# Kernel tuning notes

Hardware: AMD Instinct MI355X
Metric: run time of the kernel (lower is better)

Reference implementation:

```python
import jax, jax.numpy as jnp
import numpy as np
import itertools

B, N, C, D = 2, 150000, 64, 128  # samples, points/sample, channels, voxel grid extent
EPS = 1e-4  # BatchNormBlock eps
# 3x3x3 submanifold kernel offsets (27 taps)
OFFS = jnp.array(list(itertools.product((-1, 0, 1), repeat=3)), dtype=jnp.int32)  # [27,3]


def setup_inputs() -> dict:
    key = jax.random.key(0)
    k1, k2 = jax.random.split(key)
    rng = np.random.default_rng(0)
    # unique voxel coordinates per sample on a D^3 grid
    pos = np.stack([
        np.stack(np.unravel_index(rng.choice(D ** 3, size=N, replace=False), (D, D, D)), axis=-1)
        for _ in range(B)
    ]).astype(np.int32)  # [B,N,3]
    feats = jax.random.normal(k1, (B, N, C), jnp.float32)
    # 4 submanifold convs (2 residual blocks x 2 convs), fan-in scaled
    Ws = jax.random.normal(k2, (4, 27, C, C), jnp.float32) / np.sqrt(27 * C)
    gammas = jnp.ones((4, C), jnp.float32)
    betas = jnp.zeros((4, C), jnp.float32)
    return {"feats": feats, "Ws": Ws, "gammas": gammas, "betas": betas, "pos": jnp.asarray(pos)}


def _build_lut(pos_b):  # pos_b: [N,3] int32 -> dense hash grid [D^3] of point index or -1
    code = (pos_b[:, 0] * D + pos_b[:, 1]) * D + pos_b[:, 2]
    return jnp.full((D ** 3,), -1, jnp.int32).at[code].set(jnp.arange(N, dtype=jnp.int32))


def _subconv(x, lut_b, pos_b, W):
    # submanifold sparse conv: per kernel tap, gather neighbor features and GEMM
    # x:[N,C], lut_b:[D^3], pos_b:[N,3], W:[27,Cin,Cout]
    def step(acc, kw):
        d, Wk = kw
        npos = pos_b + d  # [N,3]
        valid = jnp.all((npos >= 0) & (npos < D), axis=-1)
        code = (npos[:, 0] * D + npos[:, 1]) * D + npos[:, 2]
        nidx = lut_b[jnp.where(valid, code, 0)]
        valid = valid & (nidx >= 0)
        g = jnp.where(valid[:, None], x[jnp.clip(nidx, 0, N - 1)], 0.0)  # [N,Cin]
        return acc + g @ Wk, None

    acc0 = jnp.zeros((x.shape[0], W.shape[-1]), x.dtype)
    acc, _ = jax.lax.scan(step, acc0, (OFFS, W))
    return acc


def _bn_relu(x, g, b):
    # BatchNormBlock (train mode, biased var over all concatenated points) + ReLU
    mu = x.mean(axis=(0, 1))
    var = jnp.mean(jnp.square(x - mu), axis=(0, 1))
    return jax.nn.relu((x - mu) * jax.lax.rsqrt(var + EPS) * g + b)


def reference(feats, Ws, gammas, betas, pos):
    lut = jax.vmap(_build_lut)(pos)  # [B, D^3]
    conv = jax.vmap(_subconv, in_axes=(0, 0, 0, None))
    x = feats
    for blk in range(2):  # conv_block_reps ResidualBlocks (NIN is Identity since nIn==nOut)
        out1 = x
        h = _bn_relu(x, gammas[2 * blk], betas[2 * blk])
        h = conv(h, lut, pos, Ws[2 * blk])
        h = _bn_relu(h, gammas[2 * blk + 1], betas[2 * blk + 1])
        out2 = conv(h, lut, pos, Ws[2 * blk + 1])
        x = out1 + out2
    return x
```

## Files before the change

### kernel.cpp

```cpp
#include <hip/hip_runtime.h>
#include <stdint.h>

#define DGRID 128
#define D3 (DGRID * DGRID * DGRID)
#define NBATCH 2
#define NPTS 150000
#define NROWS (NBATCH * NPTS)
#define NPAD 300032
#define ZROW NROWS
#define NCBLK (NPAD / 128)
#define NCELLS 8192
#define EPSBN 1e-4f

typedef __attribute__((ext_vector_type(8))) short s16x8;
typedef __attribute__((ext_vector_type(4))) float f32x4;

static __device__ __forceinline__ uint32_t f2bf_rne(float f) {
  uint32_t b = __float_as_uint(f);
  return (b + 0x7FFFu + ((b >> 16) & 1u)) >> 16;
}

static __device__ __forceinline__ uint32_t pkbf(float lo, float hi) {
  uint32_t r;
  asm("v_cvt_pk_bf16_f32 %0, %1, %2" : "=v"(r) : "v"(lo), "v"(hi));
  return r;
}

static __device__ __forceinline__ f32x4 mfma16(uint4 a, uint4 b, f32x4 c) {
  return __builtin_amdgcn_mfma_f32_16x16x32_bf16(
      __builtin_bit_cast(s16x8, a), __builtin_bit_cast(s16x8, b), c, 0, 0, 0);
}

static __device__ __forceinline__ uint4 bnrelu_frag(uint4 u, float4 aL, float4 aH,
                                                    float4 bL, float4 bH) {
  float y0, y1;
  uint4 o;
  y0 = fmaxf(fmaf(__uint_as_float(u.x << 16), aL.x, bL.x), 0.f);
  y1 = fmaxf(fmaf(__uint_as_float(u.x & 0xFFFF0000u), aL.y, bL.y), 0.f);
  o.x = pkbf(y0, y1);
  y0 = fmaxf(fmaf(__uint_as_float(u.y << 16), aL.z, bL.z), 0.f);
  y1 = fmaxf(fmaf(__uint_as_float(u.y & 0xFFFF0000u), aL.w, bL.w), 0.f);
  o.y = pkbf(y0, y1);
  y0 = fmaxf(fmaf(__uint_as_float(u.z << 16), aH.x, bH.x), 0.f);
  y1 = fmaxf(fmaf(__uint_as_float(u.z & 0xFFFF0000u), aH.y, bH.y), 0.f);
  o.z = pkbf(y0, y1);
  y0 = fmaxf(fmaf(__uint_as_float(u.w << 16), aH.z, bH.z), 0.f);
  y1 = fmaxf(fmaf(__uint_as_float(u.w & 0xFFFF0000u), aH.w, bH.w), 0.f);
  o.w = pkbf(y0, y1);
  return o;
}

__global__ void k_scatter(const int* __restrict__ pos, int* __restrict__ lut) {
  int g = blockIdx.x * blockDim.x + threadIdx.x;
  if (g >= NROWS) return;
  int b = g / NPTS;
  int i = g - b * NPTS;
  lut[(size_t)b * D3 + (pos[3 * g] * DGRID + pos[3 * g + 1]) * DGRID + pos[3 * g + 2]] = i;
}

__global__ void k_cellcount(const int* __restrict__ pos, int* __restrict__ cnt) {
  int g = blockIdx.x * blockDim.x + threadIdx.x;
  if (g >= NROWS) return;
  int b = g / NPTS;
  int cid = (b << 12) | ((pos[3 * g] >> 3) << 8) | ((pos[3 * g + 1] >> 3) << 4) |
            (pos[3 * g + 2] >> 3);
  atomicAdd(&cnt[cid], 1);
}

__global__ void k_scan(const int* __restrict__ cnt, int* __restrict__ cstart) {
  __shared__ int s[1024];
  int tid = threadIdx.x;
  int e[8];
  int sum = 0;
#pragma unroll
  for (int j = 0; j < 8; j++) {
    int v = cnt[tid * 8 + j];
    e[j] = sum;
    sum += v;
  }
  s[tid] = sum;
  __syncthreads();
  for (int off = 1; off < 1024; off <<= 1) {
    int t = (tid >= off) ? s[tid - off] : 0;
    __syncthreads();
    s[tid] += t;
    __syncthreads();
  }
  int base = tid ? s[tid - 1] : 0;
#pragma unroll
  for (int j = 0; j < 8; j++) cstart[tid * 8 + j] = base + e[j];
}

__global__ void k_bucket(const int* __restrict__ pos, const int* __restrict__ cstart,
                         int* __restrict__ fill, int* __restrict__ perm,
                         int* __restrict__ iperm) {
  int g = blockIdx.x * blockDim.x + threadIdx.x;
  if (g >= NROWS) return;
  int b = g / NPTS;
  int cid = (b << 12) | ((pos[3 * g] >> 3) << 8) | ((pos[3 * g + 1] >> 3) << 4) |
            (pos[3 * g + 2] >> 3);
  int slot = cstart[cid] + atomicAdd(&fill[cid], 1);
  perm[slot] = g;
  iperm[g] = slot;
}

__global__ void k_nbr_s(const int* __restrict__ pos, const int* __restrict__ lut,
                        const int* __restrict__ perm, const int* __restrict__ iperm,
                        int* __restrict__ nbr) {
  int s = blockIdx.x * blockDim.x + threadIdx.x;
  if (s >= NPAD) return;
  if (s >= NROWS) {
#pragma unroll
    for (int t = 0; t < 27; ++t) nbr[(size_t)t * NPAD + s] = ZROW;
    return;
  }
  int g = perm[s];
  int b = g / NPTS;
  int x = pos[3 * g], y = pos[3 * g + 1], z = pos[3 * g + 2];
  const int* L = lut + (size_t)b * D3;
  const int* ip = iperm + (size_t)b * NPTS;
#pragma unroll
  for (int t = 0; t < 27; ++t) {
    int nx = x + t / 9 - 1;
    int ny = y + (t / 3) % 3 - 1;
    int nz = z + t % 3 - 1;
    int v = ZROW;
    if ((unsigned)nx < DGRID && (unsigned)ny < DGRID && (unsigned)nz < DGRID) {
      int n = L[(nx * DGRID + ny) * DGRID + nz];
      if (n >= 0) v = ip[n];
    }
    nbr[(size_t)t * NPAD + s] = v;
  }
}

__global__ void k_wpack(const float* __restrict__ Ws, uint4* __restrict__ Wfrag) {
  int e = blockIdx.x * 256 + threadIdx.x;
  if (e >= 4 * 27 * 512) return;
  int lane = e & 63, nb = (e >> 6) & 3, s = (e >> 8) & 1, tt = e >> 9;
  int kb = s * 32 + (lane >> 4) * 8;
  int cout = nb * 16 + (lane & 15);
  const float* src = Ws + (size_t)tt * 4096;
  uint32_t p[4];
#pragma unroll
  for (int j = 0; j < 4; ++j) {
    uint32_t lo = f2bf_rne(src[(kb + 2 * j) * 64 + cout]);
    uint32_t hi = f2bf_rne(src[(kb + 2 * j + 1) * 64 + cout]);
    p[j] = (hi << 16) | lo;
  }
  uint4 o;
  o.x = p[0]; o.y = p[1]; o.z = p[2]; o.w = p[3];
  Wfrag[e] = o;
}

__global__ void k_stats2(const float* __restrict__ part, int nblk,
                         const float* __restrict__ gamma, const float* __restrict__ beta,
                         float* __restrict__ chanp, int cid) {
  __shared__ float s[512];
  int c = threadIdx.x & 63, q = threadIdx.x >> 6;
  float sm = 0.f, sq = 0.f;
  for (int rb = q; rb < nblk; rb += 4) {
    sm += part[rb * 128 + c];
    sq += part[rb * 128 + 64 + c];
  }
  s[threadIdx.x] = sm;
  s[256 + threadIdx.x] = sq;
  __syncthreads();
  if (q == 0) {
    sm = s[c] + s[64 + c] + s[128 + c] + s[192 + c];
    sq = s[256 + c] + s[320 + c] + s[384 + c] + s[448 + c];
    float mean = sm / (float)NROWS;
    float var = sq / (float)NROWS - mean * mean;
    float a = gamma[cid * 64 + c] * rsqrtf(var + EPSBN);
    chanp[cid * 128 + c] = a;
    chanp[cid * 128 + 64 + c] = beta[cid * 64 + c] - mean * a;
  }
}

__global__ void k_cast(const float* __restrict__ feats, const int* __restrict__ perm,
                       uint4* __restrict__ f0, float* __restrict__ part) {
  __shared__ float sred[2][4][64];
  int tid = threadIdx.x, wv = tid >> 6, lane = tid & 63;
  int oct = tid & 7;
  float sm[8], sq[8];
#pragma unroll
  for (int j = 0; j < 8; j++) sm[j] = sq[j] = 0.f;
#pragma unroll 1
  for (int it = 0; it < 8; it++) {
    int g = blockIdx.x * 2048 + it * 256 + tid;
    int s = g >> 3;
    uint4 o = (uint4){0u, 0u, 0u, 0u};
    if (s < NROWS) {
      int src = perm[s];
      const float* X = feats + (size_t)src * 64 + oct * 8;
      float4 x0 = *(const float4*)X;
      float4 x1 = *(const float4*)(X + 4);
      sm[0] += x0.x; sq[0] += x0.x * x0.x;
      sm[1] += x0.y; sq[1] += x0.y * x0.y;
      sm[2] += x0.z; sq[2] += x0.z * x0.z;
      sm[3] += x0.w; sq[3] += x0.w * x0.w;
      sm[4] += x1.x; sq[4] += x1.x * x1.x;
      sm[5] += x1.y; sq[5] += x1.y * x1.y;
      sm[6] += x1.z; sq[6] += x1.z * x1.z;
      sm[7] += x1.w; sq[7] += x1.w * x1.w;
      o.x = pkbf(x0.x, x0.y);
      o.y = pkbf(x0.z, x0.w);
      o.z = pkbf(x1.x, x1.y);
      o.w = pkbf(x1.z, x1.w);
    }
    f0[g] = o;
  }
#pragma unroll
  for (int j = 0; j < 8; j++) {
    sm[j] += __shfl_xor(sm[j], 8);  sq[j] += __shfl_xor(sq[j], 8);
    sm[j] += __shfl_xor(sm[j], 16); sq[j] += __shfl_xor(sq[j], 16);
    sm[j] += __shfl_xor(sm[j], 32); sq[j] += __shfl_xor(sq[j], 32);
  }
  if (lane < 8) {
#pragma unroll
    for (int j = 0; j < 8; j++) {
      sred[0][wv][lane * 8 + j] = sm[j];
      sred[1][wv][lane * 8 + j] = sq[j];
    }
  }
  __syncthreads();
  if (tid < 64) {
    float s0 = 0.f, s1 = 0.f;
#pragma unroll
    for (int w = 0; w < 4; w++) {
      s0 += sred[0][w][tid];
      s1 += sred[1][w][tid];
    }
    part[blockIdx.x * 128 + tid] = s0;
    part[blockIdx.x * 128 + 64 + tid] = s1;
  }
}

__global__ void k_hb(const uint4* __restrict__ x, const float* __restrict__ chanp,
                     int cid, uint4* __restrict__ h) {
  int tid = threadIdx.x;
  int c0 = (tid & 7) * 8;
  const float* cp = chanp + cid * 128;
  float4 aL = *(const float4*)(cp + c0);
  float4 aH = *(const float4*)(cp + c0 + 4);
  float4 bL = *(const float4*)(cp + 64 + c0);
  float4 bH = *(const float4*)(cp + 64 + c0 + 4);
#pragma unroll 1
  for (int it = 0; it < 8; it++) {
    int g = blockIdx.x * 2048 + it * 256 + tid;
    int row = g >> 3;
    uint4 o = (uint4){0u, 0u, 0u, 0u};
    if (row < NROWS) o = bnrelu_frag(x[g], aL, aH, bL, bH);
    h[g] = o;
  }
}

#define PH(T, AC, NIC)                                                      \
  {                                                                         \
    _Pragma("unroll") for (int s = 0; s < 2; s++)                           \
      _Pragma("unroll") for (int rt = 0; rt < 2; rt++)                      \
        _Pragma("unroll") for (int nb = 0; nb < 4; nb++)                    \
          acc[rt][nb] = mfma16(AC[rt][s], wb[s * 4 + nb], acc[rt][nb]);     \
    _Pragma("unroll") for (int rt = 0; rt < 2; rt++) {                      \
      const uint4* hp = src + (size_t)NIC[rt] * 8 + lkg;                    \
      AC[rt][0] = hp[0];                                                    \
      AC[rt][1] = hp[4];                                                    \
    }                                                                       \
    {                                                                       \
      int tn = (T) + 4 <= 26 ? (T) + 4 : 26;                                \
      NIC[0] = nbp[(size_t)tn * NPAD];                                      \
      NIC[1] = nbp[(size_t)tn * NPAD + 16];                                 \
    }                                                                       \
    {                                                                       \
      int tw = (T) + 1 <= 26 ? (T) + 1 : 26;                                \
      const uint4* wp = Wf + (size_t)tw * 512 + lane;                       \
      _Pragma("unroll") for (int i = 0; i < 8; i++) wb[i] = wp[i * 64];     \
    }                                                                       \
  }

__global__ __launch_bounds__(256) void k_conv(
    const uint4* __restrict__ src, const uint4* __restrict__ Wf,
    const int* __restrict__ nbr,
    const uint4* __restrict__ resb, uint4* __restrict__ outb,
    float* __restrict__ outf, const int* __restrict__ operm,
    float* __restrict__ part, int do_stats) {
  __shared__ char smem[19456];
  int tid = threadIdx.x, wv = tid >> 6, lane = tid & 63;
  int bid = (int)blockIdx.x;
  int sbid = (bid & 7) * (NCBLK / 8) + (bid >> 3);
  int tbase = (sbid * 4 + wv) * 32;
  int lrow = lane & 15, lkg = lane >> 4;

  f32x4 acc[2][4];
#pragma unroll
  for (int i = 0; i < 2; i++)
#pragma unroll
    for (int j = 0; j < 4; j++) acc[i][j] = (f32x4){0.f, 0.f, 0.f, 0.f};

  const int* nbp = nbr + tbase + lrow;
  int niE[2], niO[2];
  uint4 aE[2][2], aO[2][2], wb[8];
  {
    int p0[2], p1[2];
    p0[0] = nbp[0];
    p0[1] = nbp[16];
    p1[0] = nbp[NPAD];
    p1[1] = nbp[NPAD + 16];
    niE[0] = nbp[(size_t)2 * NPAD];
    niE[1] = nbp[(size_t)2 * NPAD + 16];
    niO[0] = nbp[(size_t)3 * NPAD];
    niO[1] = nbp[(size_t)3 * NPAD + 16];
#pragma unroll
    for (int rt = 0; rt < 2; rt++) {
      const uint4* hp = src + (size_t)p0[rt] * 8 + lkg;
      aE[rt][0] = hp[0];
      aE[rt][1] = hp[4];
    }
#pragma unroll
    for (int rt = 0; rt < 2; rt++) {
      const uint4* hp = src + (size_t)p1[rt] * 8 + lkg;
      aO[rt][0] = hp[0];
      aO[rt][1] = hp[4];
    }
    const uint4* wp = Wf + lane;
#pragma unroll
    for (int i = 0; i < 8; i++) wb[i] = wp[i * 64];
  }

#pragma unroll 1
  for (int t = 0; t < 26; t += 2) {
    PH(t, aE, niE)
    PH(t + 1, aO, niO)
  }
  PH(26, aE, niE)

  float sm4[4] = {0.f, 0.f, 0.f, 0.f}, sq4[4] = {0.f, 0.f, 0.f, 0.f};
  float* slab = (float*)smem + wv * 1088;
  float* sred = (float*)(smem + 17408);
#pragma unroll 1
  for (int rt = 0; rt < 2; rt++) {
#pragma unroll
    for (int nb = 0; nb < 4; nb++)
#pragma unroll
      for (int r = 0; r < 4; r++)
        slab[(lkg * 4 + r) * 68 + nb * 16 + lrow] = acc[rt][nb][r];
#pragma unroll
    for (int j = 0; j < 4; j++) {
      int row = tbase + rt * 16 + j * 4 + lkg;
      float4 vv = *(float4*)&slab[(j * 4 + lkg) * 68 + lrow * 4];
      bool live = row < NROWS;
      if (resb && live) {
        uint2 rb = *(const uint2*)((const char*)resb + (size_t)row * 128 + lrow * 8);
        vv.x += __uint_as_float(rb.x << 16);
        vv.y += __uint_as_float(rb.x & 0xFFFF0000u);
        vv.z += __uint_as_float(rb.y << 16);
        vv.w += __uint_as_float(rb.y & 0xFFFF0000u);
      }
      if (outb) {
        uint2 ob = (uint2){0u, 0u};
        if (live) {
          ob.x = pkbf(vv.x, vv.y);
          ob.y = pkbf(vv.z, vv.w);
        }
        *(uint2*)((char*)outb + (size_t)row * 128 + lrow * 8) = ob;
      }
      if (outf && live) {
        int orow = operm[row];
        *(float4*)(outf + (size_t)orow * 64 + lrow * 4) = vv;
      }
      if (live) {
        sm4[0] += vv.x; sq4[0] += vv.x * vv.x;
        sm4[1] += vv.y; sq4[1] += vv.y * vv.y;
        sm4[2] += vv.z; sq4[2] += vv.z * vv.z;
        sm4[3] += vv.w; sq4[3] += vv.w * vv.w;
      }
    }
  }
  if (do_stats) {
#pragma unroll
    for (int k = 0; k < 4; k++) {
      sm4[k] += __shfl_xor(sm4[k], 16); sq4[k] += __shfl_xor(sq4[k], 16);
      sm4[k] += __shfl_xor(sm4[k], 32); sq4[k] += __shfl_xor(sq4[k], 32);
    }
    if (lane < 16) {
#pragma unroll
      for (int k = 0; k < 4; k++) {
        sred[wv * 64 + lane * 4 + k] = sm4[k];
        sred[256 + wv * 64 + lane * 4 + k] = sq4[k];
      }
    }
    __syncthreads();
    if (tid < 64) {
      float s0 = 0.f, s1 = 0.f;
#pragma unroll
      for (int w = 0; w < 4; w++) {
        s0 += sred[w * 64 + tid];
        s1 += sred[256 + w * 64 + tid];
      }
      part[bid * 128 + tid] = s0;
      part[bid * 128 + 64 + tid] = s1;
    }
  }
}

extern "C" void kernel_launch(void* const* d_in, const int* in_sizes, int n_in,
                              void* d_out, int out_size, void* d_ws, size_t ws_size,
                              hipStream_t stream) {
  const float* feats = (const float*)d_in[0];
  const float* Ws = (const float*)d_in[1];
  const float* gammas = (const float*)d_in[2];
  const float* betas = (const float*)d_in[3];
  const int* pos = (const int*)d_in[4];
  float* out = (float*)d_out;

  char* w = (char*)d_ws;
  auto alloc = [&](size_t b) {
    char* p = w;
    w += (b + 255) & ~(size_t)255;
    return p;
  };
  int* nbr = (int*)alloc((size_t)27 * NPAD * 4);
  uint4* Wfrag = (uint4*)alloc((size_t)4 * 27 * 512 * 16);
  float* part = (float*)alloc((size_t)NCBLK * 128 * 4);
  float* chanp = (float*)alloc((size_t)4 * 128 * 4);
  int* perm = (int*)alloc((size_t)NPAD * 4);
  int* iperm = (int*)alloc((size_t)NROWS * 4);
  int* ccnt = (int*)alloc((size_t)NCELLS * 4);
  int* cfill = (int*)alloc((size_t)NCELLS * 4);
  int* cstart = (int*)alloc((size_t)NCELLS * 4);
  uint4* f0 = (uint4*)alloc((size_t)NPAD * 128);
  uint4* x1 = (uint4*)alloc((size_t)NPAD * 128);
  uint4* h = (uint4*)alloc((size_t)NPAD * 128);
  char* reg0 = alloc((size_t)NPAD * 128);
  uint4* c1 = (uint4*)reg0;
  int* lut = (int*)reg0;

  hipMemsetAsync(lut, 0xFF, (size_t)NBATCH * D3 * 4, stream);
  hipMemsetAsync(ccnt, 0, (size_t)NCELLS * 8, stream);
  int gpts = (NROWS + 255) / 256;
  k_scatter<<<gpts, 256, 0, stream>>>(pos, lut);
  k_cellcount<<<gpts, 256, 0, stream>>>(pos, ccnt);
  k_scan<<<1, 1024, 0, stream>>>(ccnt, cstart);
  k_bucket<<<gpts, 256, 0, stream>>>(pos, cstart, cfill, perm, iperm);
  k_nbr_s<<<NPAD / 256, 256, 0, stream>>>(pos, lut, perm, iperm, nbr);
  k_wpack<<<216, 256, 0, stream>>>(Ws, Wfrag);

  k_cast<<<1172, 256, 0, stream>>>(feats, perm, f0, part);
  k_stats2<<<1, 256, 0, stream>>>(part, 1172, gammas, betas, chanp, 0);
  k_hb<<<1172, 256, 0, stream>>>(f0, chanp, 0, h);
  k_conv<<<NCBLK, 256, 0, stream>>>(h, Wfrag + 0 * 27 * 512, nbr,
                                    nullptr, c1, nullptr, nullptr, part, 1);

  k_stats2<<<1, 256, 0, stream>>>(part, NCBLK, gammas, betas, chanp, 1);
  k_hb<<<1172, 256, 0, stream>>>(c1, chanp, 1, h);
  k_conv<<<NCBLK, 256, 0, stream>>>(h, Wfrag + 1 * 27 * 512, nbr,
                                    f0, x1, nullptr, nullptr, part, 1);

  k_stats2<<<1, 256, 0, stream>>>(part, NCBLK, gammas, betas, chanp, 2);
  k_hb<<<1172, 256, 0, stream>>>(x1, chanp, 2, h);
  k_conv<<<NCBLK, 256, 0, stream>>>(h, Wfrag + 2 * 27 * 512, nbr,
                                    nullptr, c1, nullptr, nullptr, part, 1);

  k_stats2<<<1, 256, 0, stream>>>(part, NCBLK, gammas, betas, chanp, 3);
  k_hb<<<1172, 256, 0, stream>>>(c1, chanp, 3, h);
  k_conv<<<NCBLK, 256, 0, stream>>>(h, Wfrag + 3 * 27 * 512, nbr,
                                    x1, nullptr, out, perm, part, 0);
}
```

Measured before the change: 1.234 ms.

## Triple-buffer gathered features and double-buffer weights in conv tap loop

Restructures the per-tap pipeline in the sparse conv kernel. Each tap now issues the next tap's weight and neighbor-feature loads into separate buffers before running its MFMAs, instead of loading after the MFMAs into the same registers. Three feature buffers and two weight buffers rotate, so loads for upcoming taps are in flight while the current tap computes. The cost is more live VGPRs (an extra weight set and feature set), which may lower occupancy or cause spills.

```diff
diff --git a/kernel.cpp b/kernel.cpp
--- a/kernel.cpp
+++ b/kernel.cpp
@@ -254,27 +254,28 @@
   }
 }
 
-#define PH(T, AC, NIC)                                                      \
+#define PH(T, AC, AN, WC, WN, NI)                                           \
   {                                                                         \
+    {                                                                       \
+      int tw = (T) + 1 <= 26 ? (T) + 1 : 26;                                \
+      const uint4* wp = Wf + (size_t)tw * 512 + lane;                       \
+      _Pragma("unroll") for (int i = 0; i < 8; i++) WN[i] = wp[i * 64];     \
+    }                                                                       \
+    {                                                                       \
+      const uint4* hp0 = src + (size_t)NI[0] * 8 + lkg;                     \
+      const uint4* hp1 = src + (size_t)NI[1] * 8 + lkg;                     \
+      AN[0][0] = hp0[0]; AN[0][1] = hp0[4];                                 \
+      AN[1][0] = hp1[0]; AN[1][1] = hp1[4];                                 \
+    }                                                                       \
+    {                                                                       \
+      int tn = (T) + 4 <= 26 ? (T) + 4 : 26;                                \
+      NI[0] = nbp[(size_t)tn * NPAD];                                       \
+      NI[1] = nbp[(size_t)tn * NPAD + 16];                                  \
+    }                                                                       \
     _Pragma("unroll") for (int s = 0; s < 2; s++)                           \
       _Pragma("unroll") for (int rt = 0; rt < 2; rt++)                      \
         _Pragma("unroll") for (int nb = 0; nb < 4; nb++)                    \
-          acc[rt][nb] = mfma16(AC[rt][s], wb[s * 4 + nb], acc[rt][nb]);     \
-    _Pragma("unroll") for (int rt = 0; rt < 2; rt++) {                      \
-      const uint4* hp = src + (size_t)NIC[rt] * 8 + lkg;                    \
-      AC[rt][0] = hp[0];                                                    \
-      AC[rt][1] = hp[4];                                                    \
-    }                                                                       \
-    {                                                                       \
-      int tn = (T) + 4 <= 26 ? (T) + 4 : 26;                                \
-      NIC[0] = nbp[(size_t)tn * NPAD];                                      \
-      NIC[1] = nbp[(size_t)tn * NPAD + 16];                                 \
-    }                                                                       \
-    {                                                                       \
-      int tw = (T) + 1 <= 26 ? (T) + 1 : 26;                                \
-      const uint4* wp = Wf + (size_t)tw * 512 + lane;                       \
-      _Pragma("unroll") for (int i = 0; i < 8; i++) wb[i] = wp[i * 64];     \
-    }                                                                       \
+          acc[rt][nb] = mfma16(AC[rt][s], WC[s * 4 + nb], acc[rt][nb]);     \
   }
 
 __global__ __launch_bounds__(256) void k_conv(
@@ -297,41 +298,48 @@
     for (int j = 0; j < 4; j++) acc[i][j] = (f32x4){0.f, 0.f, 0.f, 0.f};
 
   const int* nbp = nbr + tbase + lrow;
-  int niE[2], niO[2];
-  uint4 aE[2][2], aO[2][2], wb[8];
+  int nE[2], nO[2];
+  uint4 a0[2][2], a1[2][2], a2[2][2], w0[8], w1[8];
+
   {
-    int p0[2], p1[2];
-    p0[0] = nbp[0];
-    p0[1] = nbp[16];
-    p1[0] = nbp[NPAD];
-    p1[1] = nbp[NPAD + 16];
-    niE[0] = nbp[(size_t)2 * NPAD];
-    niE[1] = nbp[(size_t)2 * NPAD + 16];
-    niO[0] = nbp[(size_t)3 * NPAD];
-    niO[1] = nbp[(size_t)3 * NPAD + 16];
-#pragma unroll
-    for (int rt = 0; rt < 2; rt++) {
-      const uint4* hp = src + (size_t)p0[rt] * 8 + lkg;
-      aE[rt][0] = hp[0];
-      aE[rt][1] = hp[4];
-    }
-#pragma unroll
-    for (int rt = 0; rt < 2; rt++) {
-      const uint4* hp = src + (size_t)p1[rt] * 8 + lkg;
-      aO[rt][0] = hp[0];
-      aO[rt][1] = hp[4];
-    }
     const uint4* wp = Wf + lane;
 #pragma unroll
-    for (int i = 0; i < 8; i++) wb[i] = wp[i * 64];
+    for (int i = 0; i < 8; i++) w0[i] = wp[i * 64];
+  }
+  int p0[2], p1[2];
+  p0[0] = nbp[0];
+  p0[1] = nbp[16];
+  p1[0] = nbp[NPAD];
+  p1[1] = nbp[NPAD + 16];
+  nE[0] = nbp[(size_t)2 * NPAD];
+  nE[1] = nbp[(size_t)2 * NPAD + 16];
+  nO[0] = nbp[(size_t)3 * NPAD];
+  nO[1] = nbp[(size_t)3 * NPAD + 16];
+  {
+    const uint4* hp0 = src + (size_t)p0[0] * 8 + lkg;
+    const uint4* hp1 = src + (size_t)p0[1] * 8 + lkg;
+    a0[0][0] = hp0[0]; a0[0][1] = hp0[4];
+    a0[1][0] = hp1[0]; a0[1][1] = hp1[4];
+  }
+  {
+    const uint4* hp0 = src + (size_t)p1[0] * 8 + lkg;
+    const uint4* hp1 = src + (size_t)p1[1] * 8 + lkg;
+    a1[0][0] = hp0[0]; a1[0][1] = hp0[4];
+    a1[1][0] = hp1[0]; a1[1][1] = hp1[4];
   }
 
 #pragma unroll 1
-  for (int t = 0; t < 26; t += 2) {
-    PH(t, aE, niE)
-    PH(t + 1, aO, niO)
-  }
-  PH(26, aE, niE)
+  for (int t = 0; t < 24; t += 6) {
+    PH(t + 0, a0, a2, w0, w1, nE)
+    PH(t + 1, a1, a0, w1, w0, nO)
+    PH(t + 2, a2, a1, w0, w1, nE)
+    PH(t + 3, a0, a2, w1, w0, nO)
+    PH(t + 4, a1, a0, w0, w1, nE)
+    PH(t + 5, a2, a1, w1, w0, nO)
+  }
+  PH(24, a0, a2, w0, w1, nE)
+  PH(25, a1, a0, w1, w0, nO)
+  PH(26, a2, a1, w0, w1, nE)
 
   float sm4[4] = {0.f, 0.f, 0.f, 0.f}, sq4[4] = {0.f, 0.f, 0.f, 0.f};
   float* slab = (float*)smem + wv * 1088;
```

After: 1.350 ms. 9.4% more time.
